# Optimization experiments

Measured on AMD Instinct MI355X. Metric: run time of the kernel, lower is better.

The kernel has to match this reference:

```python
import jax, jax.numpy as jnp
import numpy as np

DECAY = 0.2
THRESH = 0.5
LENS = 0.5  # surrogate-gradient window half-width

@jax.custom_vjp
def spike(mem):
    # Heaviside spike at threshold (standard BP-SNN act_fun)
    return (mem > THRESH).astype(mem.dtype)

def _spike_fwd(mem):
    return spike(mem), mem

def _spike_bwd(mem, g):
    # rectangular surrogate gradient
    surr = (jnp.abs(mem - THRESH) < LENS).astype(mem.dtype)
    return (g * surr,)

spike.defvjp(_spike_fwd, _spike_bwd)


def setup_inputs() -> dict:
    key = jax.random.key(0)
    k1, k2, k3 = jax.random.split(key, 3)
    B, T, N_IN, N_H2, N_CLS = 2048, 50, 620, 620, 11
    x = jax.random.normal(k1, (B, T, N_IN), dtype=jnp.float32)
    # PyTorch Linear default init: U(-1/sqrt(fan_in), 1/sqrt(fan_in))
    b1 = 1.0 / np.sqrt(N_IN)
    b2 = 1.0 / np.sqrt(N_H2)
    W1 = jax.random.uniform(k2, (N_H2, N_IN), jnp.float32, -b1, b1)
    W2 = jax.random.uniform(k3, (N_CLS, N_H2), jnp.float32, -b2, b2)
    return {"x": x, "W1": W1, "W2": W2}


def reference(x, W1, W2):
    B = x.shape[0]
    T = x.shape[1]
    n_h2 = W1.shape[0]   # 620
    n_cls = W2.shape[0]  # 11

    def step(carry, xt):
        h1_mem, h1_spk, h2_mem, h2_spk, acc = carry
        # mem_update for layer 1: fc = Linear(no bias) + ReLU
        h1_mem = h1_mem * DECAY * (1.0 - h1_spk) + jax.nn.relu(xt @ W1.T)
        h1_spk = spike(h1_mem)
        # mem_update for layer 2
        h2_mem = h2_mem * DECAY * (1.0 - h2_spk) + jax.nn.relu(h1_spk @ W2.T)
        h2_spk = spike(h2_mem)
        return (h1_mem, h1_spk, h2_mem, h2_spk, acc + h2_spk), None

    z1 = jnp.zeros((B, n_h2), x.dtype)
    z2 = jnp.zeros((B, n_cls), x.dtype)
    carry0 = (z1, z1, z2, z2, z2)
    xs = jnp.swapaxes(x, 0, 1)  # [T, B, n_in]
    (_, _, _, _, sumspike), _ = jax.lax.scan(step, carry0, xs)
    return sumspike / 50.0
```

## Files before the change

kernel.cpp:

```cpp
#include <hip/hip_runtime.h>
#include <cstdint>
#include <cstddef>

#define B_TOT 2048
#define T_TOT 50
#define NIN   620
#define NH    620
#define NCLS  11

#define KC 384

#define BM 128
#define BN 128
#define KB 32

__global__ __launch_bounds__(256, 3)
void gemm_relu_kernel(const float* __restrict__ X,
                      const float* __restrict__ W1,
                      float* __restrict__ Z,
                      int t0, int ct)
{
    __shared__ float As[KB][BM + 4];
    __shared__ float Bs[KB][BN + 4];

    const int tid = threadIdx.x;
    const int n0 = blockIdx.x * BN;
    const int m0 = blockIdx.y * BM;
    const int tx = tid & 15;
    const int ty = tid >> 4;

    int a_off[4], b_off[4];
    int s_row[4], s_kl[4], b_ok[4];
#pragma unroll
    for (int it = 0; it < 4; ++it) {
        int task = tid + it * 256;
        int row  = (task >> 2) & 127;
        int kl   = (task >> 9) * 16 + (task & 3) * 4;
        s_row[it] = row;
        s_kl[it]  = kl;
        int m  = m0 + row;
        int bb = m / ct;
        int dt = m - bb * ct;
        a_off[it] = (bb * T_TOT + (t0 + dt)) * NIN + kl;
        int n = n0 + row;
        b_off[it] = n * NIN + kl;
        b_ok[it]  = (n < NH);
    }

    float acc[8][8];
#pragma unroll
    for (int i = 0; i < 8; ++i)
#pragma unroll
        for (int j = 0; j < 8; ++j) acc[i][j] = 0.0f;

    const int zc0 = n0 + tx * 4;
    const int zc1 = n0 + 64 + tx * 4;

    float4 pa[4];

#pragma unroll
    for (int it = 0; it < 4; ++it) {
        pa[it] = *(const float4*)(X + a_off[it]);
        float4 bv = make_float4(0.f, 0.f, 0.f, 0.f);
        if (b_ok[it]) bv = *(const float4*)(W1 + b_off[it]);
        As[s_kl[it] + 0][s_row[it]] = pa[it].x;
        As[s_kl[it] + 1][s_row[it]] = pa[it].y;
        As[s_kl[it] + 2][s_row[it]] = pa[it].z;
        As[s_kl[it] + 3][s_row[it]] = pa[it].w;
        Bs[s_kl[it] + 0][s_row[it]] = bv.x;
        Bs[s_kl[it] + 1][s_row[it]] = bv.y;
        Bs[s_kl[it] + 2][s_row[it]] = bv.z;
        Bs[s_kl[it] + 3][s_row[it]] = bv.w;
    }

    for (int k0 = 0; k0 < NIN; k0 += KB) {
        __syncthreads();

        const int k0n = k0 + KB;
        const bool has_next = (k0n < NIN);

        if (has_next) {
#pragma unroll
            for (int it = 0; it < 4; ++it) {
                pa[it] = make_float4(0.f, 0.f, 0.f, 0.f);
                if (k0n + s_kl[it] < NIN)
                    pa[it] = *(const float4*)(X + a_off[it] + k0n);
            }
        }

#pragma unroll 8
        for (int kk = 0; kk < KB; ++kk) {
            float a[8], b[8];
            *(float4*)&a[0] = *(const float4*)&As[kk][ty * 8];
            *(float4*)&a[4] = *(const float4*)&As[kk][ty * 8 + 4];
            *(float4*)&b[0] = *(const float4*)&Bs[kk][tx * 4];
            *(float4*)&b[4] = *(const float4*)&Bs[kk][64 + tx * 4];
#pragma unroll
            for (int i = 0; i < 8; ++i)
#pragma unroll
                for (int j = 0; j < 8; ++j)
                    acc[i][j] = fmaf(a[i], b[j], acc[i][j]);
        }

        if (k0 + KB == KC) {
#pragma unroll
            for (int i = 0; i < 8; ++i) {
                float* zr = Z + (size_t)(m0 + ty * 8 + i) * NH;
                if (zc0 < NH)
                    *(float4*)(zr + zc0) = make_float4(acc[i][0], acc[i][1],
                                                       acc[i][2], acc[i][3]);
                if (zc1 < NH)
                    *(float4*)(zr + zc1) = make_float4(acc[i][4], acc[i][5],
                                                       acc[i][6], acc[i][7]);
            }
#pragma unroll
            for (int i = 0; i < 8; ++i)
#pragma unroll
                for (int j = 0; j < 8; ++j) acc[i][j] = 0.0f;
        }

        __syncthreads();

        if (has_next) {
            float4 nb[4];
#pragma unroll
            for (int it = 0; it < 4; ++it) {
                nb[it] = make_float4(0.f, 0.f, 0.f, 0.f);
                if (b_ok[it] && (k0n + s_kl[it] < NIN))
                    nb[it] = *(const float4*)(W1 + b_off[it] + k0n);
            }
#pragma unroll
            for (int it = 0; it < 4; ++it) {
                As[s_kl[it] + 0][s_row[it]] = pa[it].x;
                As[s_kl[it] + 1][s_row[it]] = pa[it].y;
                As[s_kl[it] + 2][s_row[it]] = pa[it].z;
                As[s_kl[it] + 3][s_row[it]] = pa[it].w;
                Bs[s_kl[it] + 0][s_row[it]] = nb[it].x;
                Bs[s_kl[it] + 1][s_row[it]] = nb[it].y;
                Bs[s_kl[it] + 2][s_row[it]] = nb[it].z;
                Bs[s_kl[it] + 3][s_row[it]] = nb[it].w;
            }
        }
    }

#pragma unroll
    for (int i = 0; i < 8; ++i) {
        float* zr = Z + (size_t)(m0 + ty * 8 + i) * NH;
        if (zc0 < NH) {
            float4 p = *(const float4*)(zr + zc0);
            float4 v;
            v.x = fmaxf(__fadd_rn(p.x, acc[i][0]), 0.0f);
            v.y = fmaxf(__fadd_rn(p.y, acc[i][1]), 0.0f);
            v.z = fmaxf(__fadd_rn(p.z, acc[i][2]), 0.0f);
            v.w = fmaxf(__fadd_rn(p.w, acc[i][3]), 0.0f);
            *(float4*)(zr + zc0) = v;
        }
        if (zc1 < NH) {
            float4 p = *(const float4*)(zr + zc1);
            float4 v;
            v.x = fmaxf(__fadd_rn(p.x, acc[i][4]), 0.0f);
            v.y = fmaxf(__fadd_rn(p.y, acc[i][5]), 0.0f);
            v.z = fmaxf(__fadd_rn(p.z, acc[i][6]), 0.0f);
            v.w = fmaxf(__fadd_rn(p.w, acc[i][7]), 0.0f);
            *(float4*)(zr + zc1) = v;
        }
    }
}

#define NWAVE 4
__global__ __launch_bounds__(256)
void snn_kernel(const float* __restrict__ Z,
                const float* __restrict__ W2,
                float* __restrict__ state,
                float* __restrict__ out,
                int t0, int ct)
{
    __shared__ float W2s[NCLS][NH];
    __shared__ float Ss[NWAVE][NH];

    const int tid = threadIdx.x;
    for (int i = tid; i < NCLS * NH; i += 256)
        ((float*)W2s)[i] = W2[i];
    __syncthreads();

    const int lane = tid & 63;
    const int wv   = tid >> 6;
    const int b    = blockIdx.x * NWAVE + wv;

    float* st_h1m = state;
    float* st_h1s = state + (size_t)B_TOT * NH;
    float* st_h2m = state + (size_t)2 * B_TOT * NH;
    float* st_h2s = st_h2m + (size_t)B_TOT * NCLS;
    float* st_acc = st_h2s + (size_t)B_TOT * NCLS;

    float h1m[10], h1s[10];
    float h2m = 0.f, h2s = 0.f, acc = 0.f;

    if (t0 == 0) {
#pragma unroll
        for (int i = 0; i < 10; ++i) { h1m[i] = 0.f; h1s[i] = 0.f; }
    } else {
#pragma unroll
        for (int i = 0; i < 10; ++i) {
            int k = i * 64 + lane;
            if (k < NH) {
                h1m[i] = st_h1m[(size_t)b * NH + k];
                h1s[i] = st_h1s[(size_t)b * NH + k];
            } else { h1m[i] = 0.f; h1s[i] = 0.f; }
        }
        if (lane < NCLS) {
            h2m = st_h2m[(size_t)b * NCLS + lane];
            h2s = st_h2s[(size_t)b * NCLS + lane];
            acc = st_acc[(size_t)b * NCLS + lane];
        }
    }

    const int cls   = lane & 31;
    const int qbase = (lane < 32) ? 0 : (KC / 4);
    const int qcnt  = (lane < 32) ? (KC / 4) : ((NH - KC) / 4);

    float zr[10];
    {
        const float* z0 = Z + (size_t)b * ct * NH;
#pragma unroll
        for (int i = 0; i < 10; ++i) {
            int k = i * 64 + lane;
            zr[i] = (k < NH) ? z0[k] : 0.0f;
        }
    }

    for (int dt = 0; dt < ct; ++dt) {
#pragma unroll
        for (int i = 0; i < 10; ++i) {
            int k = i * 64 + lane;
            if (k < NH) {
                float dec = __fmul_rn(__fmul_rn(h1m[i], 0.2f), (1.0f - h1s[i]));
                float m = __fadd_rn(dec, zr[i]);
                float s = (m > 0.5f) ? 1.0f : 0.0f;
                h1m[i] = m; h1s[i] = s;
                Ss[wv][k] = s;
            }
        }
        __syncthreads();

        if (dt + 1 < ct) {
            const float* zn = Z + ((size_t)b * ct + (dt + 1)) * NH;
#pragma unroll
            for (int i = 0; i < 10; ++i) {
                int k = i * 64 + lane;
                if (k < NH) zr[i] = zn[k];
            }
        }

        float csum = 0.0f;
        if (cls < NCLS) {
            const float4* w4 = (const float4*)&W2s[cls][0] + qbase;
            const float4* s4 = (const float4*)&Ss[wv][0] + qbase;
            int q = 0;
            for (; q + 8 <= qcnt; q += 8) {
                float4 w[8], s[8];
#pragma unroll
                for (int u = 0; u < 8; ++u) { w[u] = w4[q + u]; s[u] = s4[q + u]; }
#pragma unroll
                for (int u = 0; u < 8; ++u) {
                    csum = fmaf(s[u].x, w[u].x, csum);
                    csum = fmaf(s[u].y, w[u].y, csum);
                    csum = fmaf(s[u].z, w[u].z, csum);
                    csum = fmaf(s[u].w, w[u].w, csum);
                }
            }
            for (; q < qcnt; ++q) {
                float4 w = w4[q];
                float4 s = s4[q];
                csum = fmaf(s.x, w.x, csum);
                csum = fmaf(s.y, w.y, csum);
                csum = fmaf(s.z, w.z, csum);
                csum = fmaf(s.w, w.w, csum);
            }
        }
        float csumB = __shfl_xor(csum, 32, 64);
        if (lane < NCLS) {
            float ctot = __fadd_rn(csum, csumB);
            float dec = __fmul_rn(__fmul_rn(h2m, 0.2f), (1.0f - h2s));
            float m = __fadd_rn(dec, fmaxf(ctot, 0.0f));
            float s = (m > 0.5f) ? 1.0f : 0.0f;
            h2m = m; h2s = s;
            acc = __fadd_rn(acc, s);
        }
        __syncthreads();
    }

    if (t0 + ct >= T_TOT) {
        if (lane < NCLS)
            out[(size_t)b * NCLS + lane] = __fdiv_rn(acc, 50.0f);
    } else {
#pragma unroll
        for (int i = 0; i < 10; ++i) {
            int k = i * 64 + lane;
            if (k < NH) {
                st_h1m[(size_t)b * NH + k] = h1m[i];
                st_h1s[(size_t)b * NH + k] = h1s[i];
            }
        }
        if (lane < NCLS) {
            st_h2m[(size_t)b * NCLS + lane] = h2m;
            st_h2s[(size_t)b * NCLS + lane] = h2s;
            st_acc[(size_t)b * NCLS + lane] = acc;
        }
    }
}

extern "C" void kernel_launch(void* const* d_in, const int* in_sizes, int n_in,
                              void* d_out, int out_size, void* d_ws, size_t ws_size,
                              hipStream_t stream)
{
    const float* X  = (const float*)d_in[0];
    const float* W1 = (const float*)d_in[1];
    const float* W2 = (const float*)d_in[2];
    float* out = (float*)d_out;

    const size_t state_floats = (size_t)2 * B_TOT * NH + (size_t)3 * B_TOT * NCLS;
    const size_t state_bytes  = state_floats * sizeof(float);
    const size_t bytes_per_t  = (size_t)B_TOT * NH * sizeof(float);

    size_t avail = (ws_size > state_bytes) ? (ws_size - state_bytes) : 0;
    int chunkT = (int)(avail / bytes_per_t);
    if (chunkT > T_TOT) chunkT = T_TOT;
    if (chunkT < 1) chunkT = 1;

    float* state = (float*)d_ws;
    float* Zbuf  = state + state_floats;

    for (int t0 = 0; t0 < T_TOT; t0 += chunkT) {
        int ct = (T_TOT - t0 < chunkT) ? (T_TOT - t0) : chunkT;
        dim3 ggrid((NH + BN - 1) / BN, (B_TOT * ct) / BM);
        gemm_relu_kernel<<<ggrid, 256, 0, stream>>>(X, W1, Zbuf, t0, ct);
        snn_kernel<<<dim3(B_TOT / NWAVE), 256, 0, stream>>>(Zbuf, W2, state, out, t0, ct);
    }
}
```

Baseline: 1.457 ms.

## Process two batch rows per wave in SNN kernel, pad LDS rows, raise GEMM occupancy

The SNN kernel now gives each wavefront two batch rows instead of one. Lanes 0-21 of each half-wave compute the 11-class dot products for both rows, so the fixed W2 shared-memory load is amortised over twice as many rows and fewer lanes sit idle. The shared arrays are padded (row stride 628, with a 4-float gap at index 384) to change the LDS bank mapping and keep the two half-wave K ranges aligned. The GEMM launch-bounds occupancy hint goes from 3 to 4. Per-thread register use doubles (20-element state arrays), which may reduce SNN occupancy and could cause spills under the higher GEMM bound.

```diff
diff --git a/kernel.cpp b/kernel.cpp
--- a/kernel.cpp
+++ b/kernel.cpp
@@ -14,7 +14,7 @@
 #define BN 128
 #define KB 32
 
-__global__ __launch_bounds__(256, 3)
+__global__ __launch_bounds__(256, 4)
 void gemm_relu_kernel(const float* __restrict__ X,
                       const float* __restrict__ W1,
                       float* __restrict__ Z,
@@ -167,7 +167,12 @@
     }
 }
 
-#define NWAVE 4
+#define WPB 4
+#define BPW 2
+#define BPB (WPB*BPW)
+#define SROW 628
+#define QB_B 97
+
 __global__ __launch_bounds__(256)
 void snn_kernel(const float* __restrict__ Z,
                 const float* __restrict__ W2,
@@ -175,17 +180,25 @@
                 float* __restrict__ out,
                 int t0, int ct)
 {
-    __shared__ float W2s[NCLS][NH];
-    __shared__ float Ss[NWAVE][NH];
+    __shared__ float W2s[NCLS][SROW];
+    __shared__ float Ss[WPB * BPW][SROW];
 
     const int tid = threadIdx.x;
-    for (int i = tid; i < NCLS * NH; i += 256)
-        ((float*)W2s)[i] = W2[i];
+    for (int i = tid; i < NCLS * NH; i += 256) {
+        int c = i / NH;
+        int k = i - c * NH;
+        W2s[c][k + (k >= KC ? 4 : 0)] = W2[i];
+    }
     __syncthreads();
 
     const int lane = tid & 63;
     const int wv   = tid >> 6;
-    const int b    = blockIdx.x * NWAVE + wv;
+    const int half = lane >> 5;
+    const int l5   = lane & 31;
+    const int sub  = (l5 >= NCLS) ? 1 : 0;
+    const int cls  = l5 - sub * NCLS;
+    const int lact = (l5 < 2 * NCLS);
+    const int bb   = blockIdx.x * BPB + wv * BPW;
 
     float* st_h1m = state;
     float* st_h1s = state + (size_t)B_TOT * NH;
@@ -193,69 +206,78 @@
     float* st_h2s = st_h2m + (size_t)B_TOT * NCLS;
     float* st_acc = st_h2s + (size_t)B_TOT * NCLS;
 
-    float h1m[10], h1s[10];
+    float h1m[20], h1s[20];
     float h2m = 0.f, h2s = 0.f, acc = 0.f;
 
     if (t0 == 0) {
 #pragma unroll
-        for (int i = 0; i < 10; ++i) { h1m[i] = 0.f; h1s[i] = 0.f; }
+        for (int i = 0; i < 20; ++i) { h1m[i] = 0.f; h1s[i] = 0.f; }
     } else {
+#pragma unroll
+        for (int u = 0; u < 2; ++u)
+#pragma unroll
+        for (int i = 0; i < 10; ++i) {
+            int k = i * 64 + lane;
+            int idx = u * 10 + i;
+            if (k < NH) {
+                h1m[idx] = st_h1m[(size_t)(bb + u) * NH + k];
+                h1s[idx] = st_h1s[(size_t)(bb + u) * NH + k];
+            } else { h1m[idx] = 0.f; h1s[idx] = 0.f; }
+        }
+        if (half == 0 && lact) {
+            int b2 = bb + sub;
+            h2m = st_h2m[(size_t)b2 * NCLS + cls];
+            h2s = st_h2s[(size_t)b2 * NCLS + cls];
+            acc = st_acc[(size_t)b2 * NCLS + cls];
+        }
+    }
+
+    const int qcnt = half ? ((NH - KC) / 4) : (KC / 4);
+
+    float zr[20];
+#pragma unroll
+    for (int u = 0; u < 2; ++u) {
+        const float* z0 = Z + (size_t)(bb + u) * ct * NH;
+#pragma unroll
+        for (int i = 0; i < 10; ++i) {
+            int k = i * 64 + lane;
+            zr[u * 10 + i] = (k < NH) ? z0[k] : 0.0f;
+        }
+    }
+
+    for (int dt = 0; dt < ct; ++dt) {
+#pragma unroll
+        for (int u = 0; u < 2; ++u)
 #pragma unroll
         for (int i = 0; i < 10; ++i) {
             int k = i * 64 + lane;
             if (k < NH) {
-                h1m[i] = st_h1m[(size_t)b * NH + k];
-                h1s[i] = st_h1s[(size_t)b * NH + k];
-            } else { h1m[i] = 0.f; h1s[i] = 0.f; }
-        }
-        if (lane < NCLS) {
-            h2m = st_h2m[(size_t)b * NCLS + lane];
-            h2s = st_h2s[(size_t)b * NCLS + lane];
-            acc = st_acc[(size_t)b * NCLS + lane];
-        }
-    }
-
-    const int cls   = lane & 31;
-    const int qbase = (lane < 32) ? 0 : (KC / 4);
-    const int qcnt  = (lane < 32) ? (KC / 4) : ((NH - KC) / 4);
-
-    float zr[10];
-    {
-        const float* z0 = Z + (size_t)b * ct * NH;
-#pragma unroll
-        for (int i = 0; i < 10; ++i) {
-            int k = i * 64 + lane;
-            zr[i] = (k < NH) ? z0[k] : 0.0f;
-        }
-    }
-
-    for (int dt = 0; dt < ct; ++dt) {
-#pragma unroll
-        for (int i = 0; i < 10; ++i) {
-            int k = i * 64 + lane;
-            if (k < NH) {
-                float dec = __fmul_rn(__fmul_rn(h1m[i], 0.2f), (1.0f - h1s[i]));
-                float m = __fadd_rn(dec, zr[i]);
+                int idx = u * 10 + i;
+                float dec = __fmul_rn(__fmul_rn(h1m[idx], 0.2f), (1.0f - h1s[idx]));
+                float m = __fadd_rn(dec, zr[idx]);
                 float s = (m > 0.5f) ? 1.0f : 0.0f;
-                h1m[i] = m; h1s[i] = s;
-                Ss[wv][k] = s;
+                h1m[idx] = m; h1s[idx] = s;
+                Ss[wv * BPW + u][k + (k >= KC ? 4 : 0)] = s;
             }
         }
         __syncthreads();
 
         if (dt + 1 < ct) {
-            const float* zn = Z + ((size_t)b * ct + (dt + 1)) * NH;
-#pragma unroll
-            for (int i = 0; i < 10; ++i) {
-                int k = i * 64 + lane;
-                if (k < NH) zr[i] = zn[k];
+#pragma unroll
+            for (int u = 0; u < 2; ++u) {
+                const float* zn = Z + ((size_t)(bb + u) * ct + (dt + 1)) * NH;
+#pragma unroll
+                for (int i = 0; i < 10; ++i) {
+                    int k = i * 64 + lane;
+                    if (k < NH) zr[u * 10 + i] = zn[k];
+                }
             }
         }
 
         float csum = 0.0f;
-        if (cls < NCLS) {
-            const float4* w4 = (const float4*)&W2s[cls][0] + qbase;
-            const float4* s4 = (const float4*)&Ss[wv][0] + qbase;
+        if (lact) {
+            const float4* w4 = (const float4*)&W2s[cls][0] + (half ? QB_B : 0);
+            const float4* s4 = (const float4*)&Ss[wv * BPW + sub][0] + (half ? QB_B : 0);
             int q = 0;
             for (; q + 8 <= qcnt; q += 8) {
                 float4 w[8], s[8];
@@ -279,7 +301,7 @@
             }
         }
         float csumB = __shfl_xor(csum, 32, 64);
-        if (lane < NCLS) {
+        if (half == 0 && lact) {
             float ctot = __fadd_rn(csum, csumB);
             float dec = __fmul_rn(__fmul_rn(h2m, 0.2f), (1.0f - h2s));
             float m = __fadd_rn(dec, fmaxf(ctot, 0.0f));
@@ -291,21 +313,24 @@
     }
 
     if (t0 + ct >= T_TOT) {
-        if (lane < NCLS)
-            out[(size_t)b * NCLS + lane] = __fdiv_rn(acc, 50.0f);
+        if (half == 0 && lact)
+            out[(size_t)(bb + sub) * NCLS + cls] = __fdiv_rn(acc, 50.0f);
     } else {
+#pragma unroll
+        for (int u = 0; u < 2; ++u)
 #pragma unroll
         for (int i = 0; i < 10; ++i) {
             int k = i * 64 + lane;
             if (k < NH) {
-                st_h1m[(size_t)b * NH + k] = h1m[i];
-                st_h1s[(size_t)b * NH + k] = h1s[i];
-            }
-        }
-        if (lane < NCLS) {
-            st_h2m[(size_t)b * NCLS + lane] = h2m;
-            st_h2s[(size_t)b * NCLS + lane] = h2s;
-            st_acc[(size_t)b * NCLS + lane] = acc;
+                st_h1m[(size_t)(bb + u) * NH + k] = h1m[u * 10 + i];
+                st_h1s[(size_t)(bb + u) * NH + k] = h1s[u * 10 + i];
+            }
+        }
+        if (half == 0 && lact) {
+            int b2 = bb + sub;
+            st_h2m[(size_t)b2 * NCLS + cls] = h2m;
+            st_h2s[(size_t)b2 * NCLS + cls] = h2s;
+            st_acc[(size_t)b2 * NCLS + cls] = acc;
         }
     }
 }
@@ -335,6 +360,6 @@
         int ct = (T_TOT - t0 < chunkT) ? (T_TOT - t0) : chunkT;
         dim3 ggrid((NH + BN - 1) / BN, (B_TOT * ct) / BM);
         gemm_relu_kernel<<<ggrid, 256, 0, stream>>>(X, W1, Zbuf, t0, ct);
-        snn_kernel<<<dim3(B_TOT / NWAVE), 256, 0, stream>>>(Zbuf, W2, state, out, t0, ct);
+        snn_kernel<<<dim3(B_TOT / BPB), 256, 0, stream>>>(Zbuf, W2, state, out, t0, ct);
     }
 }
```

Result: no change. 1.477 ms (+1.4%).
